# Kernel tuning notes

Measured on AMD Instinct MI355X. Metric: run time of the kernel, lower is better.

## Reference

```python
import jax, jax.numpy as jnp
import numpy as np

N, B, D, K_IN, P = 64, 256, 1792, 35, 10
EPS = 1e-5


def setup_inputs() -> dict:
    key = jax.random.key(0)
    ks = jax.random.split(key, 8)
    s_tok = 1.0 / np.sqrt(K_IN)
    s_net = 1.0 / np.sqrt(D)
    return {
        "X": jax.random.normal(ks[0], (N, B, D), dtype=jnp.float32),
        "task_id": jax.random.normal(ks[1], (B, K_IN), dtype=jnp.float32),
        # tokens: Linear(35, 10*1792)
        "W_tok": jax.random.uniform(ks[2], (P * D, K_IN), jnp.float32, -s_tok, s_tok),
        "b_tok": jax.random.uniform(ks[3], (P * D,), jnp.float32, -s_tok, s_tok),
        # ptokens: Linear(35, 1792)
        "W_ptok": jax.random.uniform(ks[4], (D, K_IN), jnp.float32, -s_tok, s_tok),
        "b_ptok": jax.random.uniform(ks[5], (D,), jnp.float32, -s_tok, s_tok),
        # LayerNorm(1792)
        "gamma": jnp.ones((D,), jnp.float32),
        "beta": jnp.zeros((D,), jnp.float32),
        # net: Linear(1792, 10)
        "W_net": jax.random.uniform(ks[6], (P, D), jnp.float32, -s_net, s_net),
        "b_net": jax.random.uniform(ks[7], (P,), jnp.float32, -s_net, s_net),
    }


def _layernorm(x, gamma, beta):
    mu = jnp.mean(x, axis=-1, keepdims=True)
    var = jnp.mean(jnp.square(x - mu), axis=-1, keepdims=True)
    return (x - mu) * jax.lax.rsqrt(var + EPS) * gamma + beta


def reference(X, task_id, W_tok, b_tok, W_ptok, b_ptok, gamma, beta, W_net, b_net):
    # ptokens(task_id): (b, D); identical across n, so compute once and broadcast.
    ptok = task_id @ W_ptok.T + b_ptok                       # (b, D)
    task_token = _layernorm(ptok[None, :, :] + X, gamma, beta)  # (n, b, D)
    # net -> sigmoid: per-token mixing weights over P prompts.
    weight = jax.nn.sigmoid(task_token @ W_net.T + b_net)    # (n, b, P)
    # tokens(task_id): (b, P, D); identical across n, broadcast in einsum.
    prompt_bank = (task_id @ W_tok.T + b_tok).reshape(B, P, D)  # (b, P, D)
    prompt = jnp.einsum("nbp,bpd->nbd", weight, prompt_bank)  # (n, b, D)
    return X + prompt
```

## Files before the change

### kernel.cpp

```cpp
#include <hip/hip_runtime.h>
#include <hip/hip_bf16.h>

#define NN 64
#define BB 256
#define DD 1792
#define KK 35
#define PP 10
#define DQ 448
#define FR 8
#define NGRP 28

__device__ __forceinline__ float group16_sum_dpp(float x) {
    asm("v_add_f32_dpp %0, %0, %0 row_shr:1 row_mask:0xf bank_mask:0xf bound_ctrl:0" : "+v"(x));
    asm("v_add_f32_dpp %0, %0, %0 row_shr:2 row_mask:0xf bank_mask:0xf bound_ctrl:0" : "+v"(x));
    asm("v_add_f32_dpp %0, %0, %0 row_shr:4 row_mask:0xf bank_mask:0xf bound_ctrl:0" : "+v"(x));
    asm("v_add_f32_dpp %0, %0, %0 row_shr:8 row_mask:0xf bank_mask:0xf bound_ctrl:0" : "+v"(x));
    return x;
}

__global__ void prep_gf(const float* __restrict__ gamma, const float* __restrict__ beta,
                        const float* __restrict__ Wnet, const float* __restrict__ bnet,
                        float* __restrict__ GF, float* __restrict__ SG, float* __restrict__ ZC) {
    const int p = blockIdx.x;
    const int tid = threadIdx.x;
    float sg = 0.f, sb = 0.f;
#pragma unroll
    for (int j = 0; j < 7; ++j) {
        int d = j * 256 + tid;
        float wv = Wnet[p * DD + d];
        float g = gamma[d] * wv;
        GF[p * DD + d] = g;
        sg += g;
        sb += beta[d] * wv;
    }
#pragma unroll
    for (int off = 32; off > 0; off >>= 1) {
        sg += __shfl_xor(sg, off);
        sb += __shfl_xor(sb, off);
    }
    __shared__ float rs[4][2];
    if ((tid & 63) == 0) { rs[tid >> 6][0] = sg; rs[tid >> 6][1] = sb; }
    __syncthreads();
    if (tid == 0) {
        float a = 0.f, c = 0.f;
#pragma unroll
        for (int w = 0; w < 4; ++w) { a += rs[w][0]; c += rs[w][1]; }
        SG[p] = a;
        ZC[p] = c + bnet[p];
    }
}

__global__ void prep_bank(const float* __restrict__ task,
                          const float* __restrict__ Wtok, const float* __restrict__ btok,
                          const float* __restrict__ Wptok, const float* __restrict__ bptok,
                          float* __restrict__ bank, float* __restrict__ ptok) {
    __shared__ float ti[32 * KK];
    const int tid = threadIdx.x;
    const int b0 = blockIdx.y * 32;
    for (int i = tid; i < 32 * KK; i += 256) ti[i] = task[b0 * KK + i];

    const int r = blockIdx.x * 256 + tid;
    const bool isbank = (r < PP * DD);
    const int rr = isbank ? r : (r - PP * DD);
    const float* __restrict__ W = isbank ? Wtok : Wptok;
    const float bias = isbank ? btok[r] : bptok[rr];

    float w[KK];
#pragma unroll
    for (int k = 0; k < KK; ++k) w[k] = W[rr * KK + k];

    __syncthreads();
#pragma unroll 1
    for (int bb = 0; bb < 32; ++bb) {
        float acc = bias;
#pragma unroll
        for (int k = 0; k < KK; ++k) acc = fmaf(ti[bb * KK + k], w[k], acc);
        const int b = b0 + bb;
        if (isbank) bank[b * (PP * DD) + r] = acc;
        else        ptok[b * DD + rr]       = acc;
    }
}

__global__ __launch_bounds__(448) void fused_kernel(
    const float* __restrict__ X, const float* __restrict__ BANK,
    const float* __restrict__ PTOK, const float* __restrict__ GF,
    const float* __restrict__ SG, const float* __restrict__ ZC,
    float* __restrict__ OUT) {
    const int tid = threadIdx.x;
    const int b = blockIdx.y;
    const int n0 = blockIdx.x * FR;

    const float4* __restrict__ X4 = (const float4*)X;
    const float4* __restrict__ B4 = (const float4*)BANK;
    const float4* __restrict__ G4 = (const float4*)GF;
    const float4* __restrict__ P4 = (const float4*)PTOK;
    float4* __restrict__ O4 = (float4*)OUT;

    __shared__ float red[FR][NGRP][12];
    __shared__ float wlds[FR][PP];

    const size_t rstride = (size_t)BB * DQ;
    const size_t idx0 = ((size_t)n0 * BB + b) * DQ + tid;

    float4 gf[PP];
#pragma unroll
    for (int p = 0; p < PP; ++p) gf[p] = G4[p * DQ + tid];
    const float4 ptk = P4[b * DQ + tid];
    float4 x[FR];
#pragma unroll
    for (int r = 0; r < FR; ++r) x[r] = X4[idx0 + (size_t)r * rstride];

    const bool writer = ((tid & 15) == 15);
    const int g = tid >> 4;

#pragma unroll
    for (int r = 0; r < FR; ++r) {
        float4 t;
        t.x = x[r].x + ptk.x; t.y = x[r].y + ptk.y;
        t.z = x[r].z + ptk.z; t.w = x[r].w + ptk.w;

        float s1 = t.x + t.y + t.z + t.w;
        float s2 = t.x * t.x;
        s2 = fmaf(t.y, t.y, s2); s2 = fmaf(t.z, t.z, s2); s2 = fmaf(t.w, t.w, s2);
        float a[PP];
#pragma unroll
        for (int p = 0; p < PP; ++p) {
            float v = t.x * gf[p].x;
            v = fmaf(t.y, gf[p].y, v);
            v = fmaf(t.z, gf[p].z, v);
            v = fmaf(t.w, gf[p].w, v);
            a[p] = v;
        }
        s1 = group16_sum_dpp(s1);
        s2 = group16_sum_dpp(s2);
#pragma unroll
        for (int p = 0; p < PP; ++p) a[p] = group16_sum_dpp(a[p]);

        if (writer) {
            float4* dst = (float4*)&red[r][g][0];
            dst[0] = make_float4(s1, s2, a[0], a[1]);
            dst[1] = make_float4(a[2], a[3], a[4], a[5]);
            dst[2] = make_float4(a[6], a[7], a[8], a[9]);
        }
    }

    float4 bk[PP];
#pragma unroll
    for (int p = 0; p < PP; ++p) bk[p] = B4[((size_t)b * PP + p) * DQ + tid];

    __syncthreads();

    if (tid < FR * 16) {
        const int row = tid >> 4;
        const int v = tid & 15;
        float f = 0.f;
        if (v < 12) {
#pragma unroll
            for (int q = 0; q < NGRP; ++q) f += red[row][q][v];
        }
        const int base = (tid & 63) & ~15;
        const float mu = __shfl(f, base)     * (1.0f / (float)DD);
        const float ms = __shfl(f, base + 1) * (1.0f / (float)DD);
        const float istd = rsqrtf(ms - mu * mu + 1e-5f);
        if (v >= 2 && v < 12) {
            const int p = v - 2;
            const float z = istd * (f - mu * SG[p]) + ZC[p];
            wlds[row][p] = 1.0f / (1.0f + __expf(-z));
        }
    }
    __syncthreads();

#pragma unroll
    for (int r = 0; r < FR; ++r) {
        float4 acc = x[r];
#pragma unroll
        for (int p = 0; p < PP; ++p) {
            const float wv = wlds[r][p];
            acc.x = fmaf(wv, bk[p].x, acc.x);
            acc.y = fmaf(wv, bk[p].y, acc.y);
            acc.z = fmaf(wv, bk[p].z, acc.z);
            acc.w = fmaf(wv, bk[p].w, acc.w);
        }
        O4[idx0 + (size_t)r * rstride] = acc;
    }
}

extern "C" void kernel_launch(void* const* d_in, const int* in_sizes, int n_in,
                              void* d_out, int out_size, void* d_ws, size_t ws_size,
                              hipStream_t stream) {
    const float* X     = (const float*)d_in[0];
    const float* task  = (const float*)d_in[1];
    const float* Wtok  = (const float*)d_in[2];
    const float* btok  = (const float*)d_in[3];
    const float* Wptok = (const float*)d_in[4];
    const float* bptok = (const float*)d_in[5];
    const float* gamma = (const float*)d_in[6];
    const float* beta  = (const float*)d_in[7];
    const float* Wnet  = (const float*)d_in[8];
    const float* bnet  = (const float*)d_in[9];
    float* out = (float*)d_out;

    float* ws = (float*)d_ws;
    float* bank = ws;
    float* ptok = bank + (size_t)BB * PP * DD;
    float* GF   = ptok + (size_t)BB * DD;
    float* SG   = GF + PP * DD;
    float* ZC   = SG + PP;

    prep_gf<<<PP, 256, 0, stream>>>(gamma, beta, Wnet, bnet, GF, SG, ZC);
    prep_bank<<<dim3(77, 8), 256, 0, stream>>>(task, Wtok, btok, Wptok, bptok, bank, ptok);
    fused_kernel<<<dim3(NN / FR, BB), 448, 0, stream>>>(X, bank, ptok, GF, SG, ZC, out);
}
```

Before: 90.12 us.

## Restructure fused kernel so each wave owns whole rows, reducing without LDS

The fused kernel now assigns four n-rows of one batch entry to each wavefront, walking the 1792-wide feature dimension in seven 64-lane chunks. Statistics and the ten projections are reduced across the wave with DPP and shuffles, which removes the shared-memory reduction and both block barriers. The trade-off is that X is read twice (once for the statistics pass and again for the output pass), relying on L2 hits, and the grid becomes 1024 blocks of 256 threads. Chunked loads are software-prefetched one chunk ahead.

```diff
diff --git a/kernel.cpp b/kernel.cpp
--- a/kernel.cpp
+++ b/kernel.cpp
@@ -7,8 +7,8 @@
 #define KK 35
 #define PP 10
 #define DQ 448
-#define FR 8
-#define NGRP 28
+#define RPW 4
+#define CH 7
 
 __device__ __forceinline__ float group16_sum_dpp(float x) {
     asm("v_add_f32_dpp %0, %0, %0 row_shr:1 row_mask:0xf bank_mask:0xf bound_ctrl:0" : "+v"(x));
@@ -16,6 +16,13 @@
     asm("v_add_f32_dpp %0, %0, %0 row_shr:4 row_mask:0xf bank_mask:0xf bound_ctrl:0" : "+v"(x));
     asm("v_add_f32_dpp %0, %0, %0 row_shr:8 row_mask:0xf bank_mask:0xf bound_ctrl:0" : "+v"(x));
     return x;
+}
+
+__device__ __forceinline__ float wave_allsum(float x) {
+    x = group16_sum_dpp(x);
+    x += __shfl_xor(x, 16);
+    x += __shfl_xor(x, 32);
+    return __shfl(x, 63);
 }
 
 __global__ void prep_gf(const float* __restrict__ gamma, const float* __restrict__ beta,
@@ -81,14 +88,18 @@
     }
 }
 
-__global__ __launch_bounds__(448) void fused_kernel(
+__global__ __launch_bounds__(256) void fused_wave(
     const float* __restrict__ X, const float* __restrict__ BANK,
     const float* __restrict__ PTOK, const float* __restrict__ GF,
     const float* __restrict__ SG, const float* __restrict__ ZC,
     float* __restrict__ OUT) {
-    const int tid = threadIdx.x;
-    const int b = blockIdx.y;
-    const int n0 = blockIdx.x * FR;
+    const int tid  = threadIdx.x;
+    const int lane = tid & 63;
+    const int wid  = tid >> 6;
+    const int bid  = blockIdx.x;
+    const int b    = bid & (BB - 1);
+    const int item = ((bid >> 8) << 2) + wid;
+    const int n0   = item * RPW;
 
     const float4* __restrict__ X4 = (const float4*)X;
     const float4* __restrict__ B4 = (const float4*)BANK;
@@ -96,92 +107,99 @@
     const float4* __restrict__ P4 = (const float4*)PTOK;
     float4* __restrict__ O4 = (float4*)OUT;
 
-    __shared__ float red[FR][NGRP][12];
-    __shared__ float wlds[FR][PP];
-
-    const size_t rstride = (size_t)BB * DQ;
-    const size_t idx0 = ((size_t)n0 * BB + b) * DQ + tid;
-
-    float4 gf[PP];
-#pragma unroll
-    for (int p = 0; p < PP; ++p) gf[p] = G4[p * DQ + tid];
-    const float4 ptk = P4[b * DQ + tid];
-    float4 x[FR];
-#pragma unroll
-    for (int r = 0; r < FR; ++r) x[r] = X4[idx0 + (size_t)r * rstride];
-
-    const bool writer = ((tid & 15) == 15);
-    const int g = tid >> 4;
-
-#pragma unroll
-    for (int r = 0; r < FR; ++r) {
-        float4 t;
-        t.x = x[r].x + ptk.x; t.y = x[r].y + ptk.y;
-        t.z = x[r].z + ptk.z; t.w = x[r].w + ptk.w;
-
-        float s1 = t.x + t.y + t.z + t.w;
-        float s2 = t.x * t.x;
-        s2 = fmaf(t.y, t.y, s2); s2 = fmaf(t.z, t.z, s2); s2 = fmaf(t.w, t.w, s2);
-        float a[PP];
+    const size_t rstr = (size_t)BB * DQ;
+    const size_t x0   = ((size_t)n0 * BB + b) * DQ + lane;
+    const size_t pb   = (size_t)b * DQ + lane;
+
+    float acc[RPW][12];
+#pragma unroll
+    for (int r = 0; r < RPW; ++r)
+#pragma unroll
+        for (int v = 0; v < 12; ++v) acc[r][v] = 0.f;
+
+    float4 xv[2][RPW];
+#pragma unroll
+    for (int r = 0; r < RPW; ++r) xv[0][r] = X4[x0 + (size_t)r * rstr];
+
+#pragma unroll
+    for (int c = 0; c < CH; ++c) {
+        const int cur = c & 1, nxt = cur ^ 1;
+        float4 gfv[PP];
+#pragma unroll
+        for (int p = 0; p < PP; ++p) gfv[p] = G4[(size_t)p * DQ + c * 64 + lane];
+        const float4 pt = P4[pb + c * 64];
+        if (c < CH - 1) {
+#pragma unroll
+            for (int r = 0; r < RPW; ++r)
+                xv[nxt][r] = X4[x0 + (c + 1) * 64 + (size_t)r * rstr];
+        }
+#pragma unroll
+        for (int r = 0; r < RPW; ++r) {
+            const float tx = xv[cur][r].x + pt.x;
+            const float ty = xv[cur][r].y + pt.y;
+            const float tz = xv[cur][r].z + pt.z;
+            const float tw = xv[cur][r].w + pt.w;
+            acc[r][0] += tx + ty + tz + tw;
+            float s2 = fmaf(tx, tx, acc[r][1]);
+            s2 = fmaf(ty, ty, s2); s2 = fmaf(tz, tz, s2); s2 = fmaf(tw, tw, s2);
+            acc[r][1] = s2;
+#pragma unroll
+            for (int p = 0; p < PP; ++p) {
+                float v = fmaf(tx, gfv[p].x, acc[r][2 + p]);
+                v = fmaf(ty, gfv[p].y, v);
+                v = fmaf(tz, gfv[p].z, v);
+                v = fmaf(tw, gfv[p].w, v);
+                acc[r][2 + p] = v;
+            }
+        }
+    }
+
+#pragma unroll
+    for (int r = 0; r < RPW; ++r)
+#pragma unroll
+        for (int v = 0; v < 12; ++v) acc[r][v] = wave_allsum(acc[r][v]);
+
+    float wgt[RPW][PP];
+#pragma unroll
+    for (int r = 0; r < RPW; ++r) {
+        const float mu   = acc[r][0] * (1.0f / (float)DD);
+        const float ms   = acc[r][1] * (1.0f / (float)DD);
+        const float istd = rsqrtf(ms - mu * mu + 1e-5f);
 #pragma unroll
         for (int p = 0; p < PP; ++p) {
-            float v = t.x * gf[p].x;
-            v = fmaf(t.y, gf[p].y, v);
-            v = fmaf(t.z, gf[p].z, v);
-            v = fmaf(t.w, gf[p].w, v);
-            a[p] = v;
-        }
-        s1 = group16_sum_dpp(s1);
-        s2 = group16_sum_dpp(s2);
-#pragma unroll
-        for (int p = 0; p < PP; ++p) a[p] = group16_sum_dpp(a[p]);
-
-        if (writer) {
-            float4* dst = (float4*)&red[r][g][0];
-            dst[0] = make_float4(s1, s2, a[0], a[1]);
-            dst[1] = make_float4(a[2], a[3], a[4], a[5]);
-            dst[2] = make_float4(a[6], a[7], a[8], a[9]);
-        }
-    }
-
-    float4 bk[PP];
-#pragma unroll
-    for (int p = 0; p < PP; ++p) bk[p] = B4[((size_t)b * PP + p) * DQ + tid];
-
-    __syncthreads();
-
-    if (tid < FR * 16) {
-        const int row = tid >> 4;
-        const int v = tid & 15;
-        float f = 0.f;
-        if (v < 12) {
-#pragma unroll
-            for (int q = 0; q < NGRP; ++q) f += red[row][q][v];
-        }
-        const int base = (tid & 63) & ~15;
-        const float mu = __shfl(f, base)     * (1.0f / (float)DD);
-        const float ms = __shfl(f, base + 1) * (1.0f / (float)DD);
-        const float istd = rsqrtf(ms - mu * mu + 1e-5f);
-        if (v >= 2 && v < 12) {
-            const int p = v - 2;
-            const float z = istd * (f - mu * SG[p]) + ZC[p];
-            wlds[row][p] = 1.0f / (1.0f + __expf(-z));
-        }
-    }
-    __syncthreads();
-
-#pragma unroll
-    for (int r = 0; r < FR; ++r) {
-        float4 acc = x[r];
-#pragma unroll
-        for (int p = 0; p < PP; ++p) {
-            const float wv = wlds[r][p];
-            acc.x = fmaf(wv, bk[p].x, acc.x);
-            acc.y = fmaf(wv, bk[p].y, acc.y);
-            acc.z = fmaf(wv, bk[p].z, acc.z);
-            acc.w = fmaf(wv, bk[p].w, acc.w);
-        }
-        O4[idx0 + (size_t)r * rstride] = acc;
+            const float z = istd * (acc[r][2 + p] - mu * SG[p]) + ZC[p];
+            wgt[r][p] = 1.0f / (1.0f + __expf(-z));
+        }
+    }
+
+    const size_t bb0 = (size_t)b * PP * DQ + lane;
+    float4 x2[2][RPW];
+#pragma unroll
+    for (int r = 0; r < RPW; ++r) x2[0][r] = X4[x0 + (size_t)r * rstr];
+
+#pragma unroll
+    for (int c = 0; c < CH; ++c) {
+        const int cur = c & 1, nxt = cur ^ 1;
+        float4 bk[PP];
+#pragma unroll
+        for (int p = 0; p < PP; ++p) bk[p] = B4[bb0 + (size_t)p * DQ + c * 64];
+        if (c < CH - 1) {
+#pragma unroll
+            for (int r = 0; r < RPW; ++r)
+                x2[nxt][r] = X4[x0 + (c + 1) * 64 + (size_t)r * rstr];
+        }
+#pragma unroll
+        for (int r = 0; r < RPW; ++r) {
+            float4 o = x2[cur][r];
+#pragma unroll
+            for (int p = 0; p < PP; ++p) {
+                o.x = fmaf(wgt[r][p], bk[p].x, o.x);
+                o.y = fmaf(wgt[r][p], bk[p].y, o.y);
+                o.z = fmaf(wgt[r][p], bk[p].z, o.z);
+                o.w = fmaf(wgt[r][p], bk[p].w, o.w);
+            }
+            O4[x0 + c * 64 + (size_t)r * rstr] = o;
+        }
     }
 }
 
@@ -209,5 +227,5 @@
 
     prep_gf<<<PP, 256, 0, stream>>>(gamma, beta, Wnet, bnet, GF, SG, ZC);
     prep_bank<<<dim3(77, 8), 256, 0, stream>>>(task, Wtok, btok, Wptok, bptok, bank, ptok);
-    fused_kernel<<<dim3(NN / FR, BB), 448, 0, stream>>>(X, bank, ptok, GF, SG, ZC, out);
-}
+    fused_wave<<<1024, 256, 0, stream>>>(X, bank, ptok, GF, SG, ZC, out);
+}
```

Result: slower. 114.5 us (+27.0%).
